# Performance work log

Hardware: AMD Instinct MI355X
Metric: run time of the kernel (lower is better)

Reference implementation:

```python
import jax, jax.numpy as jnp
import numpy as np

B, T, V, F, H, WIN = 512, 49, 34, 16, 64, 4
W = T - WIN + 1  # 46 sliding windows


def make_pe(max_len, d):
    pos = np.arange(max_len, dtype=np.float32)[:, None]
    div = np.exp(np.arange(0, d, 2, dtype=np.float32) * (-np.log(10000.0) / d))
    pe = np.zeros((max_len, d), dtype=np.float32)
    pe[:, 0::2] = np.sin(pos * div)
    pe[:, 1::2] = np.cos(pos * div)
    return jnp.asarray(pe)


def impute(arr, delta_ts, mask, w, b):
    # arr/mask [B,T,V], delta_ts [B,T]; serial masked cumulative-sum + LOCF scan
    missing = (mask == 0).astype(arr.dtype)
    dd = jnp.broadcast_to(delta_ts[:, :, None], arr.shape)

    def step(carry, inp):
        c_prev, x_prev = carry
        d_t, x_t, m_t = inp
        c_t = d_t + c_prev * m_t                      # cum delta resets at observations
        x_new = jnp.where(m_t > 0, x_prev, x_t)       # last-observation carry-forward
        return (c_t, x_new), (c_t, x_new)

    xs = (dd.swapaxes(0, 1)[1:], arr.swapaxes(0, 1)[1:], missing.swapaxes(0, 1)[1:])
    _, (c_rest, x_rest) = jax.lax.scan(step, (dd[:, 0], arr[:, 0]), xs)
    cum = jnp.concatenate([dd[:, :1], c_rest.swapaxes(0, 1)], axis=1)
    last = jnp.concatenate([arr[:, :1], x_rest.swapaxes(0, 1)], axis=1)
    cum = cum / jnp.max(cum)
    decay = jnp.exp(-jnp.clip(w * cum + b, 0.0, 1000.0))  # w,b broadcast [1,V]
    means = jnp.mean(arr, axis=1, keepdims=True)
    return arr * mask + (1 - mask) * (decay * last + (1 - decay) * means)


def gru_layer(x, Wih, Whh, bih, bhh):
    # torch GRU gate order r,z,n; Wih [in,3H], Whh [H,3H]
    nB = x.shape[0]
    Hh = Whh.shape[0]
    xW = x @ Wih + bih  # [B,T,3H] precomputed input projections

    def step(h, xw_t):
        gh = h @ Whh + bhh
        xr, xz, xn = jnp.split(xw_t, 3, axis=-1)
        hr, hz, hn = jnp.split(gh, 3, axis=-1)
        r = jax.nn.sigmoid(xr + hr)
        z = jax.nn.sigmoid(xz + hz)
        n = jnp.tanh(xn + r * hn)
        h_new = (1 - z) * n + z * h
        return h_new, h_new

    _, ys = jax.lax.scan(step, jnp.zeros((nB, Hh), x.dtype), xW.swapaxes(0, 1))
    return ys.swapaxes(0, 1)


def forward(arr, mask, time, w_input_decay, b_input_decay,
            enc_W1, enc_b1, enc_W2, enc_b2,
            tla_Wq, tla_bq, tla_Wk, tla_bk, tla_Wv, tla_bv,
            adj, mp_W1, mp_b1, mp_W2, mp_b2,
            sa_Wq, sa_bq, sa_Wk, sa_bk, sa_Wv, sa_bv,
            gru_Wih0, gru_Whh0, gru_bih0, gru_bhh0,
            gru_Wih1, gru_Whh1, gru_bih1, gru_bhh1,
            ta_Wq, ta_bq, ta_Wk, ta_bk, ta_Wv, ta_bv,
            cls_W1, cls_b1, cls_W2, cls_b2):
    tt = time.T  # [B,T]
    delta = jnp.concatenate([jnp.zeros((tt.shape[0], 1), tt.dtype), tt[:, 1:] - tt[:, :-1]], axis=1)
    x = impute(arr, delta, mask, w_input_decay, b_input_decay)  # [B,T,V]
    # per-variable 2-layer MLP encoders (batched over V via einsum)
    inp = jnp.stack([x, mask], axis=-1)  # [B,T,V,2]
    h = jax.nn.relu(jnp.einsum('btvi,vif->btvf', inp, enc_W1) + enc_b1)
    enc = jnp.einsum('btvf,vfg->btvg', h, enc_W2) + enc_b2  # [B,T,V,F]
    # sliding windows (torch unfold + permute) + window positional encoding
    idx = jnp.arange(W)[:, None] + jnp.arange(WIN)[None, :]
    win = enc[:, idx] + make_pe(WIN, F)[None, None, :, None, :]
    xw = win.reshape(B * W, WIN, V, F)
    # TimeLagAttentionLayer: separate attention per variable, batched via einsum
    q = jnp.einsum('blvf,vfg->blvg', xw, tla_Wq) + tla_bq
    k = jnp.einsum('blvf,vfg->blvg', xw, tla_Wk) + tla_bk
    v = jnp.einsum('blvf,vfg->blvg', xw, tla_Wv) + tla_bv
    scores = jnp.einsum('blvg,bmvg->bvlm', q, k) / jnp.sqrt(jnp.asarray(F, xw.dtype))
    att = jax.nn.softmax(scores, axis=-1)
    att_out = jnp.einsum('bvlm,bmvf->bvf', att, v)  # (att @ v) then sum over lag dim
    # MessagePassingLayer
    message = jnp.einsum('uv,bvf->buf', adj, att_out)
    mp_out = jax.nn.relu(message @ mp_W1 + mp_b1) @ mp_W2 + mp_b2  # [B*W,V,1] (t_out path)
    _ = mp_out
    latent = message
    l_out = latent.reshape(B, W, V, F).transpose(0, 2, 3, 1)  # [B,V,F,W]
    # SignalAttentionLayer (faithful: permute to [B,V,W,F] then raw reshape to [B*W,V,F])
    xs = l_out + make_pe(V, F)[None, :, :, None]
    xs = xs.transpose(0, 1, 3, 2).reshape(B * W, V, F)
    Q = xs @ sa_Wq + sa_bq
    K = xs @ sa_Wk + sa_bk
    Vv = xs @ sa_Wv + sa_bv
    sw = jax.nn.softmax(jnp.einsum('bnd,bmd->bnm', Q, K) / jnp.sqrt(jnp.asarray(F, xs.dtype)), axis=-1)
    s_out = jnp.einsum('bnm,bmd->bd', sw, Vv).reshape(B, W, F)  # (w @ V).sum(dim=1)
    # 2-layer GRU predictor
    g1 = gru_layer(s_out, gru_Wih0, gru_Whh0, gru_bih0, gru_bhh0)
    g2 = gru_layer(g1, gru_Wih1, gru_Whh1, gru_bih1, gru_bhh1)  # [B,W,H]
    # TemporalAttention pooling
    xt = g2 + make_pe(W, H)[None]
    Qt = xt @ ta_Wq + ta_bq
    Kt = xt @ ta_Wk + ta_bk
    Vt = xt @ ta_Wv + ta_bv
    tw = jax.nn.softmax(jnp.einsum('bld,bmd->blm', Qt, Kt) / jnp.sqrt(jnp.asarray(H, xt.dtype)), axis=-1)
    t_val = jnp.einsum('blm,bmd->bd', tw, Vt)  # [B,H]
    pred = jax.nn.relu(t_val @ cls_W1 + cls_b1) @ cls_W2 + cls_b2  # [B,1]
    return pred


def setup_inputs():
    key = jax.random.key(0)
    ks = jax.random.split(key, 48)

    def rn(k, shape, s=0.1):
        return jax.random.normal(k, shape, jnp.float32) * s

    d = {}
    d['arr'] = jax.random.normal(ks[0], (B, T, V), jnp.float32)
    d['mask'] = (jax.random.uniform(ks[1], (B, T, V)) < 0.7).astype(jnp.float32)
    d['time'] = jnp.cumsum(jax.random.uniform(ks[2], (T, B), jnp.float32), axis=0)
    d['w_input_decay'] = jnp.full((1, V), 0.1, jnp.float32)
    d['b_input_decay'] = jnp.zeros((1, V), jnp.float32)
    d['enc_W1'] = rn(ks[3], (V, 2, F), 0.5); d['enc_b1'] = rn(ks[4], (V, F))
    d['enc_W2'] = rn(ks[5], (V, F, F), 0.25); d['enc_b2'] = rn(ks[6], (V, F))
    d['tla_Wq'] = rn(ks[7], (V, F, F), 0.25); d['tla_bq'] = rn(ks[8], (V, F))
    d['tla_Wk'] = rn(ks[9], (V, F, F), 0.25); d['tla_bk'] = rn(ks[10], (V, F))
    d['tla_Wv'] = rn(ks[11], (V, F, F), 0.25); d['tla_bv'] = rn(ks[12], (V, F))
    d['adj'] = jnp.eye(V, dtype=jnp.float32) + 0.2 * jnp.ones((V, V), jnp.float32)
    d['mp_W1'] = rn(ks[13], (F, F), 0.25); d['mp_b1'] = rn(ks[14], (F,))
    d['mp_W2'] = rn(ks[15], (F, 1), 0.25); d['mp_b2'] = rn(ks[16], (1,))
    d['sa_Wq'] = rn(ks[17], (F, F), 0.25); d['sa_bq'] = rn(ks[18], (F,))
    d['sa_Wk'] = rn(ks[19], (F, F), 0.25); d['sa_bk'] = rn(ks[20], (F,))
    d['sa_Wv'] = rn(ks[21], (F, F), 0.25); d['sa_bv'] = rn(ks[22], (F,))
    d['gru_Wih0'] = rn(ks[23], (F, 3 * H), 0.2); d['gru_Whh0'] = rn(ks[24], (H, 3 * H), 0.1)
    d['gru_bih0'] = rn(ks[25], (3 * H,)); d['gru_bhh0'] = rn(ks[26], (3 * H,))
    d['gru_Wih1'] = rn(ks[27], (H, 3 * H), 0.1); d['gru_Whh1'] = rn(ks[28], (H, 3 * H), 0.1)
    d['gru_bih1'] = rn(ks[29], (3 * H,)); d['gru_bhh1'] = rn(ks[30], (3 * H,))
    d['ta_Wq'] = rn(ks[31], (H, H), 0.12); d['ta_bq'] = rn(ks[32], (H,))
    d['ta_Wk'] = rn(ks[33], (H, H), 0.12); d['ta_bk'] = rn(ks[34], (H,))
    d['ta_Wv'] = rn(ks[35], (H, H), 0.12); d['ta_bv'] = rn(ks[36], (H,))
    d['cls_W1'] = rn(ks[37], (H, H), 0.12); d['cls_b1'] = rn(ks[38], (H,))
    d['cls_W2'] = rn(ks[39], (H, 1), 0.12); d['cls_b2'] = rn(ks[40], (1,))
    return d


def reference(arr, mask, time, w_input_decay, b_input_decay,
              enc_W1, enc_b1, enc_W2, enc_b2,
              tla_Wq, tla_bq, tla_Wk, tla_bk, tla_Wv, tla_bv,
              adj, mp_W1, mp_b1, mp_W2, mp_b2,
              sa_Wq, sa_bq, sa_Wk, sa_bk, sa_Wv, sa_bv,
              gru_Wih0, gru_Whh0, gru_bih0, gru_bhh0,
              gru_Wih1, gru_Whh1, gru_bih1, gru_bhh1,
              ta_Wq, ta_bq, ta_Wk, ta_bk, ta_Wv, ta_bv,
              cls_W1, cls_b1, cls_W2, cls_b2):
    return forward(arr, mask, time, w_input_decay, b_input_decay,
                   enc_W1, enc_b1, enc_W2, enc_b2,
                   tla_Wq, tla_bq, tla_Wk, tla_bk, tla_Wv, tla_bv,
                   adj, mp_W1, mp_b1, mp_W2, mp_b2,
                   sa_Wq, sa_bq, sa_Wk, sa_bk, sa_Wv, sa_bv,
                   gru_Wih0, gru_Whh0, gru_bih0, gru_bhh0,
                   gru_Wih1, gru_Whh1, gru_bih1, gru_bhh1,
                   ta_Wq, ta_bq, ta_Wk, ta_bk, ta_Wv, ta_bv,
                   cls_W1, cls_b1, cls_W2, cls_b2)
```

## Files before the change

### kernel.cpp

```cpp
#include <hip/hip_runtime.h>
#include <math.h>

#define BB 512
#define TT 49
#define VV 34
#define FF 16
#define HH 64
#define WW 46
#define BW (BB*WW)
#define TH3 (3*HH)
#define ROWS 25088

#define SOUT_OFF   0ull
#define XW1_OFF    376832ull
#define G1_OFF     (XW1_OFF + 4521984ull)
#define XW2_OFF    (G1_OFF + 1507328ull)
#define G2_OFF     (XW2_OFF + 4521984ull)

#define MSG_SZ     12812288ull
#define CUM_SZ     852992ull
#define MEANS_SZ   17408ull
#define AO_OFF     12435456ull
#define MSG2_OFF   (AO_OFF + MSG_SZ)
#define CUM2_OFF   (MSG2_OFF + MSG_SZ)
#define LAST2_OFF  (CUM2_OFF + CUM_SZ)
#define MEANS2_OFF (LAST2_OFF + CUM_SZ)
#define MAX2_OFF   (MEANS2_OFF + MEANS_SZ)
#define PQ_OFF     (MAX2_OFF + 4ull)
#define SAW_OFF    (PQ_OFF + 6528ull)
#define FW_OFF     (SAW_OFF + 292ull)
#define WVIH_OFF   (FW_OFF + 27744ull)
#define BIAS2_OFF  (WVIH_OFF + 3072ull)

__global__ __launch_bounds__(256) void k_scan(
    const float* __restrict__ arr, const float* __restrict__ msk,
    const float* __restrict__ timeTB,
    float* __restrict__ cum, float* __restrict__ last,
    float* __restrict__ means, unsigned int* __restrict__ maxv) {
  int tid = blockIdx.x * 256 + threadIdx.x;
  int b = tid / VV, v = tid - b * VV;
  const int base = b * TT * VV + v;
  float x = arr[base];
  float c = 0.f, lm = 0.f, s = x;
  cum[base] = 0.f;
  last[base] = x;
  float tp = timeTB[b];
  for (int t = 1; t < TT; ++t) {
    float tc = timeTB[t * BB + b];
    float d = tc - tp; tp = tc;
    int e = base + t * VV;
    float a = arr[e], m = msk[e];
    float miss = (m == 0.f) ? 1.f : 0.f;
    c = d + c * miss;
    x = (miss > 0.f) ? x : a;
    cum[e] = c; last[e] = x;
    lm = fmaxf(lm, c);
    s += a;
  }
  means[tid] = s * (1.f / 49.f);
  #pragma unroll
  for (int off = 32; off; off >>= 1) lm = fmaxf(lm, __shfl_xor(lm, off));
  if ((threadIdx.x & 63) == 0) atomicMax(maxv, __float_as_uint(lm));
}

__global__ __launch_bounds__(256) void k_prep(
    const float* __restrict__ tlaWq, const float* __restrict__ tlaWk,
    const float* __restrict__ tlaWv,
    const float* __restrict__ tlaBq, const float* __restrict__ tlaBk,
    const float* __restrict__ tlaBv,
    const float* __restrict__ saWq, const float* __restrict__ saBq,
    const float* __restrict__ saWk, const float* __restrict__ saBk,
    const float* __restrict__ saWv, const float* __restrict__ saBv,
    const float* __restrict__ encW2, const float* __restrict__ encB2,
    const float* __restrict__ Wih0, const float* __restrict__ bih0,
    float* __restrict__ pqg, float* __restrict__ saw, float* __restrict__ fw,
    float* __restrict__ wvih, float* __restrict__ bias2) {
  const int bid = blockIdx.x;
  const int t = threadIdx.x;
  if (bid < 26) {
    int idx = bid * 256 + t;
    if (idx >= 6528) return;
    int which = idx / 2176;
    int r = idx - which * 2176;
    int l = r / 544;
    int rr = r - l * 544;
    int v = rr >> 4, f = rr & 15;
    const float* W = which == 0 ? tlaWq : which == 1 ? tlaWk : tlaWv;
    float acc = 0.f;
    #pragma unroll
    for (int i = 0; i < FF; ++i) {
      int i2 = i & ~1;
      float dv = expf(-logf(10000.f) * (float)i2 / (float)FF);
      float ang = (float)l * dv;
      float pe = (i & 1) ? cosf(ang) : sinf(ang);
      acc += pe * W[v * 256 + i * 16 + f];
    }
    pqg[idx] = acc;
  } else if (bid == 26) {
    int i = t & 15, j = t >> 4;
    float a = 0.f;
    #pragma unroll
    for (int f = 0; f < 16; ++f) a += saWq[i * 16 + f] * saWk[j * 16 + f];
    saw[j * 16 + i] = a;
    if (t < 16) {
      float pp = 0.f, qq = 0.f;
      #pragma unroll
      for (int f = 0; f < 16; ++f) { pp += saWq[t * 16 + f] * saBk[f]; qq += saWk[t * 16 + f] * saBq[f]; }
      saw[256 + t] = pp;
      saw[272 + t] = qq;
    }
    if (t == 0) {
      float c = 0.f;
      #pragma unroll
      for (int f = 0; f < 16; ++f) c += saBq[f] * saBk[f];
      saw[288] = c;
    }
  } else if (bid < 61) {
    const int v = bid - 27;
    const int f = t >> 4, o = t & 15;
    const float* W2v = encW2 + v * 256;
    float cq = 0.f, ck = 0.f, cv = 0.f;
    #pragma unroll
    for (int g = 0; g < 16; ++g) {
      float w2 = W2v[f * 16 + g];
      cq += w2 * tlaWq[v * 256 + g * 16 + o];
      ck += w2 * tlaWk[v * 256 + g * 16 + o];
      cv += w2 * tlaWv[v * 256 + g * 16 + o];
    }
    fw[v * 816 + 0 * 272 + f * 16 + o] = cq;
    fw[v * 816 + 1 * 272 + f * 16 + o] = ck;
    fw[v * 816 + 2 * 272 + f * 16 + o] = cv;
    if (t < 48) {
      int which = t >> 4, o2 = t & 15;
      const float* Wp = which == 0 ? tlaWq : which == 1 ? tlaWk : tlaWv;
      const float* Bp = which == 0 ? tlaBq : which == 1 ? tlaBk : tlaBv;
      float acc = Bp[v * 16 + o2];
      #pragma unroll
      for (int g = 0; g < 16; ++g) acc += encB2[v * 16 + g] * Wp[v * 256 + g * 16 + o2];
      fw[v * 816 + which * 272 + 256 + o2] = acc;
    }
  } else if (bid < 73) {
    int idx = (bid - 61) * 256 + t;
    int i = idx / 192, o = idx - i * 192;
    float acc = 0.f;
    #pragma unroll
    for (int f = 0; f < 16; ++f) acc += saWv[i * 16 + f] * Wih0[f * 192 + o];
    wvih[idx] = acc;
  } else {
    if (t < 192) {
      float acc = bih0[t];
      #pragma unroll
      for (int f = 0; f < 16; ++f) acc += 34.f * saBv[f] * Wih0[f * 192 + t];
      bias2[t] = acc;
    }
  }
}

__global__ __launch_bounds__(256) void k_enc4(
    const float* __restrict__ arr, const float* __restrict__ msk,
    const float* __restrict__ cum, const float* __restrict__ last,
    const float* __restrict__ means, const unsigned int* __restrict__ maxv,
    const float* __restrict__ wdec, const float* __restrict__ bdec,
    const float* __restrict__ W1, const float* __restrict__ B1,
    const float* __restrict__ fw, const float* __restrict__ pqg,
    float* __restrict__ ao) {
  __shared__ __align__(16) float pkv[4][3][TT * 20];
  const int v = blockIdx.x % VV;
  const int bgrp = blockIdx.x / VV;
  const int tid = threadIdx.x;
  const int wave = tid >> 6, lane = tid & 63;
  const int b = bgrp * 4 + wave;
  const float* fv = fw + v * 816;
  if (lane < TT) {
    const int t = lane;
    const int idx = (b * TT + t) * VV + v;
    float inv = 1.f / __uint_as_float(*maxv);
    float a = arr[idx], m = msk[idx];
    float cc = cum[idx] * inv;
    float ttc = fminf(fmaxf(wdec[v] * cc + bdec[v], 0.f), 1000.f);
    float dec = expf(-ttc);
    float xx = a * m + (1.f - m) * (dec * last[idx] + (1.f - dec) * means[b * VV + v]);
    float h[16];
    #pragma unroll
    for (int f = 0; f < 16; ++f)
      h[f] = fmaxf(xx * W1[v * 32 + f] + m * W1[v * 32 + 16 + f] + B1[v * 16 + f], 0.f);
    #pragma unroll
    for (int which = 0; which < 3; ++which) {
      const float* C = fv + which * 272;
      float ac[16];
      #pragma unroll
      for (int g = 0; g < 16; ++g) {
        float acc = C[256 + g];
        #pragma unroll
        for (int f = 0; f < 16; ++f) acc += h[f] * C[f * 16 + g];
        ac[g] = acc;
      }
      float4* dst = (float4*)&pkv[wave][which][t * 20];
      dst[0] = make_float4(ac[0], ac[1], ac[2], ac[3]);
      dst[1] = make_float4(ac[4], ac[5], ac[6], ac[7]);
      dst[2] = make_float4(ac[8], ac[9], ac[10], ac[11]);
      dst[3] = make_float4(ac[12], ac[13], ac[14], ac[15]);
    }
  }
  __syncthreads();
  if (lane < WW) {
    const int w = lane;
    const float* P = &pkv[wave][0][0];
    const float* K = &pkv[wave][1][0];
    const float* Vp = &pkv[wave][2][0];
    float kk[4][16];
    #pragma unroll
    for (int m = 0; m < 4; ++m) {
      const float4* Kr = (const float4*)&K[(w + m) * 20];
      float4 k0 = Kr[0], k1 = Kr[1], k2 = Kr[2], k3 = Kr[3];
      const float* pq = &pqg[2176 + m * 544 + v * 16];
      kk[m][0]=k0.x+pq[0]; kk[m][1]=k0.y+pq[1]; kk[m][2]=k0.z+pq[2]; kk[m][3]=k0.w+pq[3];
      kk[m][4]=k1.x+pq[4]; kk[m][5]=k1.y+pq[5]; kk[m][6]=k1.z+pq[6]; kk[m][7]=k1.w+pq[7];
      kk[m][8]=k2.x+pq[8]; kk[m][9]=k2.y+pq[9]; kk[m][10]=k2.z+pq[10]; kk[m][11]=k2.w+pq[11];
      kk[m][12]=k3.x+pq[12]; kk[m][13]=k3.y+pq[13]; kk[m][14]=k3.z+pq[14]; kk[m][15]=k3.w+pq[15];
    }
    float sc[4][4];
    #pragma unroll
    for (int l = 0; l < 4; ++l) {
      float qv[16];
      const float4* Pr = (const float4*)&P[(w + l) * 20];
      float4 p0 = Pr[0], p1 = Pr[1], p2 = Pr[2], p3 = Pr[3];
      const float* pq = &pqg[l * 544 + v * 16];
      qv[0]=p0.x+pq[0]; qv[1]=p0.y+pq[1]; qv[2]=p0.z+pq[2]; qv[3]=p0.w+pq[3];
      qv[4]=p1.x+pq[4]; qv[5]=p1.y+pq[5]; qv[6]=p1.z+pq[6]; qv[7]=p1.w+pq[7];
      qv[8]=p2.x+pq[8]; qv[9]=p2.y+pq[9]; qv[10]=p2.z+pq[10]; qv[11]=p2.w+pq[11];
      qv[12]=p3.x+pq[12]; qv[13]=p3.y+pq[13]; qv[14]=p3.z+pq[14]; qv[15]=p3.w+pq[15];
      #pragma unroll
      for (int m = 0; m < 4; ++m) {
        float s = 0.f;
        #pragma unroll
        for (int i = 0; i < 16; ++i) s += qv[i] * kk[m][i];
        sc[l][m] = s * 0.25f;
      }
    }
    float csum[4] = {0.f, 0.f, 0.f, 0.f};
    #pragma unroll
    for (int l = 0; l < 4; ++l) {
      float mx = fmaxf(fmaxf(sc[l][0], sc[l][1]), fmaxf(sc[l][2], sc[l][3]));
      float sum = 0.f;
      #pragma unroll
      for (int m = 0; m < 4; ++m) { sc[l][m] = expf(sc[l][m] - mx); sum += sc[l][m]; }
      float r = 1.f / sum;
      #pragma unroll
      for (int m = 0; m < 4; ++m) csum[m] += sc[l][m] * r;
    }
    float outv[16];
    #pragma unroll
    for (int f = 0; f < 16; ++f) outv[f] = 0.f;
    #pragma unroll
    for (int m = 0; m < 4; ++m) {
      float c = csum[m];
      const float4* Vr = (const float4*)&Vp[(w + m) * 20];
      float4 v0 = Vr[0], v1 = Vr[1], v2 = Vr[2], v3 = Vr[3];
      const float* pq = &pqg[2 * 2176 + m * 544 + v * 16];
      outv[0] += c*(v0.x+pq[0]); outv[1] += c*(v0.y+pq[1]); outv[2] += c*(v0.z+pq[2]); outv[3] += c*(v0.w+pq[3]);
      outv[4] += c*(v1.x+pq[4]); outv[5] += c*(v1.y+pq[5]); outv[6] += c*(v1.z+pq[6]); outv[7] += c*(v1.w+pq[7]);
      outv[8] += c*(v2.x+pq[8]); outv[9] += c*(v2.y+pq[9]); outv[10] += c*(v2.z+pq[10]); outv[11] += c*(v2.w+pq[11]);
      outv[12] += c*(v3.x+pq[12]); outv[13] += c*(v3.y+pq[13]); outv[14] += c*(v3.z+pq[14]); outv[15] += c*(v3.w+pq[15]);
    }
    float4* d4 = (float4*)(ao + ((size_t)(b * VV + v) * WW + w) * 16);
    #pragma unroll
    for (int j = 0; j < 4; ++j)
      d4[j] = make_float4(outv[4*j], outv[4*j+1], outv[4*j+2], outv[4*j+3]);
  }
}

#define MPW 12
__global__ __launch_bounds__(256) void k_mp(
    const float* __restrict__ ao, const float* __restrict__ adj,
    float* __restrict__ msg2) {
  __shared__ float adjs[VV * VV];
  __shared__ __align__(16) float aos[VV][MPW * 16];
  __shared__ float pes[VV * 16];
  const int bb = blockIdx.x >> 2;
  const int wt = blockIdx.x & 3;
  const int w0 = wt * MPW;
  const int wc = (wt == 3) ? (WW - 3 * MPW) : MPW;
  const int tid = threadIdx.x;
  for (int i = tid; i < VV * VV; i += 256) adjs[i] = adj[i];
  for (int i = tid; i < VV * 16; i += 256) {
    int u = i >> 4, f = i & 15;
    int f2 = f & ~1;
    float dv = expf(-logf(10000.f) * (float)f2 / 16.f);
    float ang = (float)u * dv;
    pes[i] = (f & 1) ? cosf(ang) : sinf(ang);
  }
  const int nq = wc * 4;
  for (int i = tid; i < VV * nq; i += 256) {
    int vv2 = i / nq, r = i - vv2 * nq;
    int wl = r >> 2, q = r & 3;
    float4 val = *(const float4*)(ao + ((size_t)(bb * VV + vv2) * WW + w0 + wl) * 16 + q * 4);
    *(float4*)&aos[vv2][wl * 16 + q * 4] = val;
  }
  __syncthreads();
  for (int i = tid; i < VV * nq; i += 256) {
    int u = i / nq, r = i - u * nq;
    int wl = r >> 2, q = r & 3;
    float a0 = 0.f, a1 = 0.f, a2 = 0.f, a3 = 0.f;
    for (int vv2 = 0; vv2 < VV; ++vv2) {
      float a = adjs[u * VV + vv2];
      float4 s = *(const float4*)&aos[vv2][wl * 16 + q * 4];
      a0 += a * s.x; a1 += a * s.y; a2 += a * s.z; a3 += a * s.w;
    }
    float4 o = make_float4(a0 + pes[u * 16 + q * 4],
                           a1 + pes[u * 16 + q * 4 + 1],
                           a2 + pes[u * 16 + q * 4 + 2],
                           a3 + pes[u * 16 + q * 4 + 3]);
    *(float4*)(msg2 + ((size_t)(bb * VV + u) * WW + w0 + wl) * 16 + q * 4) = o;
  }
}

#define RL(x,i) __uint_as_float(__builtin_amdgcn_readlane(__float_as_uint(x), (i)))
__global__ __launch_bounds__(256) void k_sa6(
    const float* __restrict__ msg2, const float* __restrict__ saw,
    const float* __restrict__ wvih, const float* __restrict__ bias2,
    float* __restrict__ xw1) {
  __shared__ __align__(16) float xs[4][VV * 20];
  __shared__ float esc[4][VV * 35];
  __shared__ float csL[4][VV];
  __shared__ __align__(16) float ybL[4][16];
  const int tid = threadIdx.x;
  const int g = tid >> 6, lane = tid & 63;
  const int n = blockIdx.x * 4 + g;
  {
    const float4* src = (const float4*)(msg2 + (size_t)blockIdx.x * 4 * 544);
    for (int i = tid; i < 544; i += 256) {
      int gg = i / 136, r = i - gg * 136;
      int m = r >> 2, q = r & 3;
      ((float4*)&xs[gg][m * 20])[q] = src[i];
    }
  }
  __syncthreads();
  float x[16];
  float w = 0.f;
  if (lane < VV) {
    const float4* xr = (const float4*)&xs[g][lane * 20];
    float4 a0 = xr[0], a1 = xr[1], a2 = xr[2], a3 = xr[3];
    x[0]=a0.x; x[1]=a0.y; x[2]=a0.z; x[3]=a0.w;
    x[4]=a1.x; x[5]=a1.y; x[6]=a1.z; x[7]=a1.w;
    x[8]=a2.x; x[9]=a2.y; x[10]=a2.z; x[11]=a2.w;
    x[12]=a3.x; x[13]=a3.y; x[14]=a3.z; x[15]=a3.w;
    float z[16];
    float u = 0.f;
    #pragma unroll
    for (int j = 0; j < 16; ++j) {
      float acc = 0.f;
      #pragma unroll
      for (int i = 0; i < 16; ++i) acc += saw[j * 16 + i] * x[i];
      z[j] = acc;
    }
    #pragma unroll
    for (int i = 0; i < 16; ++i) { u += saw[256 + i] * x[i]; w += saw[272 + i] * x[i]; }
    const float c0 = saw[288] + u;
    float e[VV];
    #pragma unroll
    for (int m = 0; m < VV; ++m) {
      float p0 = 0.f, p1 = 0.f, p2 = 0.f, p3 = 0.f;
      #pragma unroll
      for (int i = 0; i < 16; i += 4) {
        p0 += z[i]     * RL(x[i], m);
        p1 += z[i + 1] * RL(x[i + 1], m);
        p2 += z[i + 2] * RL(x[i + 2], m);
        p3 += z[i + 3] * RL(x[i + 3], m);
      }
      e[m] = (((p0 + p1) + (p2 + p3)) + RL(w, m) + c0) * 0.25f;
    }
    float mx = e[0];
    #pragma unroll
    for (int m = 1; m < VV; ++m) mx = fmaxf(mx, e[m]);
    float sum = 0.f;
    #pragma unroll
    for (int m = 0; m < VV; ++m) { e[m] = expf(e[m] - mx); sum += e[m]; }
    float rr = 1.f / sum;
    #pragma unroll
    for (int m = 0; m < VV; ++m) esc[g][lane * 35 + m] = e[m] * rr;
  }
  __syncthreads();
  if (lane < VV) {
    float cs = 0.f;
    #pragma unroll
    for (int l = 0; l < VV; ++l) cs += esc[g][l * 35 + lane];
    csL[g][lane] = cs;
  }
  __syncthreads();
  if (lane < 16) {
    float acc = 0.f;
    #pragma unroll
    for (int m = 0; m < VV; ++m) acc += csL[g][m] * xs[g][m * 20 + lane];
    ybL[g][lane] = acc;
  }
  __syncthreads();
  {
    const float4* yr = (const float4*)&ybL[g][0];
    float4 y0 = yr[0], y1 = yr[1], y2 = yr[2], y3 = yr[3];
    float yv[16];
    yv[0]=y0.x; yv[1]=y0.y; yv[2]=y0.z; yv[3]=y0.w;
    yv[4]=y1.x; yv[5]=y1.y; yv[6]=y1.z; yv[7]=y1.w;
    yv[8]=y2.x; yv[9]=y2.y; yv[10]=y2.z; yv[11]=y2.w;
    yv[12]=y3.x; yv[13]=y3.y; yv[14]=y3.z; yv[15]=y3.w;
    #pragma unroll
    for (int k = 0; k < 3; ++k) {
      int o = lane + k * 64;
      float acc = bias2[o];
      #pragma unroll
      for (int i = 0; i < 16; ++i) acc += yv[i] * wvih[i * 192 + o];
      xw1[(size_t)n * 192 + o] = acc;
    }
  }
}

__global__ __launch_bounds__(64) void k_gru2(
    const float* __restrict__ xw, const float* __restrict__ Whh,
    const float* __restrict__ bhh, float* __restrict__ gout) {
  const int tid = threadIdx.x;
  const int b = blockIdx.x;
  float wr[64], wz[64], wn[64];
  #pragma unroll
  for (int i = 0; i < 64; ++i) {
    wr[i] = Whh[i * 192 + tid];
    wz[i] = Whh[i * 192 + 64 + tid];
    wn[i] = Whh[i * 192 + 128 + tid];
  }
  const float br = bhh[tid], bz = bhh[64 + tid], bn = bhh[128 + tid];
  float h = 0.f;
  const float* xr = xw + (size_t)b * WW * 192;
  for (int w = 0; w < WW; ++w, xr += 192) {
    float xrv = xr[tid], xzv = xr[64 + tid], xnv = xr[128 + tid];
    float pr0 = br, pr1 = 0.f, pr2 = 0.f, pr3 = 0.f;
    float pz0 = bz, pz1 = 0.f, pz2 = 0.f, pz3 = 0.f;
    float pn0 = bn, pn1 = 0.f, pn2 = 0.f, pn3 = 0.f;
    #pragma unroll
    for (int i = 0; i < 64; i += 4) {
      float h0 = RL(h, i), h1 = RL(h, i + 1), h2 = RL(h, i + 2), h3 = RL(h, i + 3);
      pr0 += h0 * wr[i];     pr1 += h1 * wr[i + 1];
      pr2 += h2 * wr[i + 2]; pr3 += h3 * wr[i + 3];
      pz0 += h0 * wz[i];     pz1 += h1 * wz[i + 1];
      pz2 += h2 * wz[i + 2]; pz3 += h3 * wz[i + 3];
      pn0 += h0 * wn[i];     pn1 += h1 * wn[i + 1];
      pn2 += h2 * wn[i + 2]; pn3 += h3 * wn[i + 3];
    }
    float ar = (pr0 + pr1) + (pr2 + pr3);
    float az = (pz0 + pz1) + (pz2 + pz3);
    float an = (pn0 + pn1) + (pn2 + pn3);
    float r = 1.f / (1.f + expf(-(xrv + ar)));
    float z = 1.f / (1.f + expf(-(xzv + az)));
    float n = tanhf(xnv + r * an);
    h = (1.f - z) * n + z * h;
    gout[((size_t)b * WW + w) * HH + tid] = h;
  }
}

__global__ __launch_bounds__(192) void k_xw2(
    const float* __restrict__ x, const float* __restrict__ Wih,
    const float* __restrict__ bih, float* __restrict__ xw) {
  __shared__ float xsh[16][HH];
  int n0 = blockIdx.x * 16;
  int tid = threadIdx.x;
  for (int idx = tid; idx < 16 * HH; idx += 192) {
    int ns = idx >> 6, i = idx & 63;
    xsh[ns][i] = x[(size_t)(n0 + ns) * HH + i];
  }
  __syncthreads();
  float acc[16];
  float bb = bih[tid];
  #pragma unroll
  for (int ns = 0; ns < 16; ++ns) acc[ns] = bb;
  for (int i = 0; i < HH; ++i) {
    float wv = Wih[i * TH3 + tid];
    #pragma unroll
    for (int ns = 0; ns < 16; ++ns) acc[ns] += xsh[ns][i] * wv;
  }
  #pragma unroll
  for (int ns = 0; ns < 16; ++ns) xw[(size_t)(n0 + ns) * TH3 + tid] = acc[ns];
}

__global__ __launch_bounds__(256) void k_ta(
    const float* __restrict__ g2,
    const float* __restrict__ Wq, const float* __restrict__ bq,
    const float* __restrict__ Wk, const float* __restrict__ bk,
    const float* __restrict__ Wv, const float* __restrict__ bv,
    const float* __restrict__ cW1, const float* __restrict__ cb1,
    const float* __restrict__ cW2, const float* __restrict__ cb2,
    float* __restrict__ out) {
  __shared__ float xt[WW * 65];
  __shared__ float QKVs[3][WW * 65];
  __shared__ float sc[WW * WW];
  __shared__ float cs[WW];
  __shared__ float tval[HH];
  __shared__ float hrelu[HH];
  int tid = threadIdx.x;
  int b = blockIdx.x;
  for (int idx = tid; idx < WW * HH; idx += 256) {
    int w = idx >> 6, d = idx & 63;
    int f2 = d & ~1;
    float dv = expf(-logf(10000.f) * (float)f2 / (float)HH);
    float ang = (float)w * dv;
    float pe = (d & 1) ? cosf(ang) : sinf(ang);
    xt[w * 65 + d] = g2[(size_t)(b * WW + w) * HH + d] + pe;
  }
  __syncthreads();
  if (tid < 192) {
    int which = tid >> 6, d = tid & 63;
    const float* Wt = which == 0 ? Wq : which == 1 ? Wk : Wv;
    float bias = (which == 0 ? bq : which == 1 ? bk : bv)[d];
    float col[HH];
    #pragma unroll
    for (int i = 0; i < HH; ++i) col[i] = Wt[i * HH + d];
    float* dst = &QKVs[which][0];
    for (int w = 0; w < WW; ++w) {
      float acc = bias;
      #pragma unroll
      for (int i = 0; i < HH; ++i) acc += xt[w * 65 + i] * col[i];
      dst[w * 65 + d] = acc;
    }
  }
  __syncthreads();
  for (int idx = tid; idx < WW * WW; idx += 256) {
    int l = idx / WW, m = idx - l * WW;
    float s = 0.f;
    #pragma unroll
    for (int i = 0; i < HH; ++i) s += QKVs[0][l * 65 + i] * QKVs[1][m * 65 + i];
    sc[idx] = s * 0.125f;
  }
  __syncthreads();
  if (tid < WW) {
    float mx = -1e30f;
    for (int m = 0; m < WW; ++m) mx = fmaxf(mx, sc[tid * WW + m]);
    float sum = 0.f;
    for (int m = 0; m < WW; ++m) { float e = expf(sc[tid * WW + m] - mx); sc[tid * WW + m] = e; sum += e; }
    float r = 1.f / sum;
    for (int m = 0; m < WW; ++m) sc[tid * WW + m] *= r;
  }
  __syncthreads();
  if (tid < WW) {
    float s = 0.f;
    for (int l = 0; l < WW; ++l) s += sc[l * WW + tid];
    cs[tid] = s;
  }
  __syncthreads();
  if (tid < HH) {
    float acc = 0.f;
    for (int m = 0; m < WW; ++m) acc += cs[m] * QKVs[2][m * 65 + tid];
    tval[tid] = acc;
  }
  __syncthreads();
  if (tid < HH) {
    float acc = cb1[tid];
    #pragma unroll
    for (int d = 0; d < HH; ++d) acc += tval[d] * cW1[d * HH + tid];
    hrelu[tid] = fmaxf(acc, 0.f);
  }
  __syncthreads();
  if (tid == 0) {
    float acc = cb2[0];
    for (int j = 0; j < HH; ++j) acc += hrelu[j] * cW2[j];
    out[b] = acc;
  }
}

extern "C" void kernel_launch(void* const* d_in, const int* in_sizes, int n_in,
                              void* d_out, int out_size, void* d_ws, size_t ws_size,
                              hipStream_t stream) {
  (void)in_sizes; (void)n_in; (void)out_size; (void)ws_size;
  const float* arr    = (const float*)d_in[0];
  const float* msk    = (const float*)d_in[1];
  const float* timeTB = (const float*)d_in[2];
  const float* wdec   = (const float*)d_in[3];
  const float* bdec   = (const float*)d_in[4];
  const float* encW1  = (const float*)d_in[5];
  const float* encB1  = (const float*)d_in[6];
  const float* encW2  = (const float*)d_in[7];
  const float* encB2  = (const float*)d_in[8];
  const float* tlaWq  = (const float*)d_in[9];
  const float* tlaBq  = (const float*)d_in[10];
  const float* tlaWk  = (const float*)d_in[11];
  const float* tlaBk  = (const float*)d_in[12];
  const float* tlaWv  = (const float*)d_in[13];
  const float* tlaBv  = (const float*)d_in[14];
  const float* adj    = (const float*)d_in[15];
  const float* saWq   = (const float*)d_in[20];
  const float* saBq   = (const float*)d_in[21];
  const float* saWk   = (const float*)d_in[22];
  const float* saBk   = (const float*)d_in[23];
  const float* saWv   = (const float*)d_in[24];
  const float* saBv   = (const float*)d_in[25];
  const float* gWih0  = (const float*)d_in[26];
  const float* gWhh0  = (const float*)d_in[27];
  const float* gBih0  = (const float*)d_in[28];
  const float* gBhh0  = (const float*)d_in[29];
  const float* gWih1  = (const float*)d_in[30];
  const float* gWhh1  = (const float*)d_in[31];
  const float* gBih1  = (const float*)d_in[32];
  const float* gBhh1  = (const float*)d_in[33];
  const float* taWq   = (const float*)d_in[34];
  const float* taBq   = (const float*)d_in[35];
  const float* taWk   = (const float*)d_in[36];
  const float* taBk   = (const float*)d_in[37];
  const float* taWv   = (const float*)d_in[38];
  const float* taBv   = (const float*)d_in[39];
  const float* cW1    = (const float*)d_in[40];
  const float* cb1    = (const float*)d_in[41];
  const float* cW2    = (const float*)d_in[42];
  const float* cb2    = (const float*)d_in[43];
  float* out = (float*)d_out;
  float* ws  = (float*)d_ws;

  float* ao    = ws + AO_OFF;
  float* msg2  = ws + MSG2_OFF;
  float* cum   = ws + CUM2_OFF;
  float* last  = ws + LAST2_OFF;
  float* means = ws + MEANS2_OFF;
  unsigned int* maxv = (unsigned int*)(ws + MAX2_OFF);
  float* pqg   = ws + PQ_OFF;
  float* saw   = ws + SAW_OFF;
  float* fw    = ws + FW_OFF;
  float* wvih  = ws + WVIH_OFF;
  float* bias2 = ws + BIAS2_OFF;

  float* xw1  = ws + XW1_OFF;
  float* g1   = ws + G1_OFF;
  float* xw2  = ws + XW2_OFF;
  float* g2   = ws + G2_OFF;

  hipMemsetAsync(maxv, 0, sizeof(unsigned int), stream);
  k_scan<<<68, 256, 0, stream>>>(arr, msk, timeTB, cum, last, means, maxv);
  k_prep<<<74, 256, 0, stream>>>(tlaWq, tlaWk, tlaWv, tlaBq, tlaBk, tlaBv,
                                 saWq, saBq, saWk, saBk, saWv, saBv,
                                 encW2, encB2, gWih0, gBih0,
                                 pqg, saw, fw, wvih, bias2);
  k_enc4<<<VV * 128, 256, 0, stream>>>(arr, msk, cum, last, means, maxv,
                                       wdec, bdec, encW1, encB1, fw, pqg, ao);
  k_mp<<<BB * 4, 256, 0, stream>>>(ao, adj, msg2);
  k_sa6<<<BW / 4, 256, 0, stream>>>(msg2, saw, wvih, bias2, xw1);
  k_gru2<<<BB, 64, 0, stream>>>(xw1, gWhh0, gBhh0, g1);
  k_xw2<<<BW / 16, 192, 0, stream>>>(g1, gWih1, gBih1, xw2);
  k_gru2<<<BB, 64, 0, stream>>>(xw2, gWhh1, gBhh1, g2);
  k_ta<<<BB, 256, 0, stream>>>(g2, taWq, taBq, taWk, taBk, taWv, taBv,
                               cW1, cb1, cW2, cb2, out);
}
```

Measured before the change: 345.8 us.

## Register-tile adjacency matmul, use LDS in self-attention, fast GRU activations

Message passing now transposes and pads the adjacency matrix in shared memory so each thread computes a 4x4 block of outputs, reusing both loaded operands across four accumulators. The self-attention kernel drops the readlane broadcast in favour of float4 reads from shared memory, plus an extra barrier to share per-node terms. The GRU kernel replaces expf/tanhf with __expf-based sigmoid and tanh. These aim to cut shared-memory traffic and transcendental cost, at a small cost in accuracy and some lost parallelism in the message-passing loop.

```diff
diff --git a/kernel.cpp b/kernel.cpp
--- a/kernel.cpp
+++ b/kernel.cpp
@@ -31,6 +31,13 @@
 #define FW_OFF     (SAW_OFF + 292ull)
 #define WVIH_OFF   (FW_OFF + 27744ull)
 #define BIAS2_OFF  (WVIH_OFF + 3072ull)
+
+#define RL(x,i) __uint_as_float(__builtin_amdgcn_readlane(__float_as_uint(x), (i)))
+__device__ __forceinline__ float fsig(float x) { return 1.f / (1.f + __expf(-x)); }
+__device__ __forceinline__ float ftanh(float x) {
+  float t = __expf(2.f * x);
+  return 1.f - 2.f / (t + 1.f);
+}
 
 __global__ __launch_bounds__(256) void k_scan(
     const float* __restrict__ arr, const float* __restrict__ msk,
@@ -271,10 +278,10 @@
 }
 
 #define MPW 12
-__global__ __launch_bounds__(256) void k_mp(
+__global__ __launch_bounds__(256) void k_mp2(
     const float* __restrict__ ao, const float* __restrict__ adj,
     float* __restrict__ msg2) {
-  __shared__ float adjs[VV * VV];
+  __shared__ __align__(16) float adjT[VV][36];
   __shared__ __align__(16) float aos[VV][MPW * 16];
   __shared__ float pes[VV * 16];
   const int bb = blockIdx.x >> 2;
@@ -282,7 +289,10 @@
   const int w0 = wt * MPW;
   const int wc = (wt == 3) ? (WW - 3 * MPW) : MPW;
   const int tid = threadIdx.x;
-  for (int i = tid; i < VV * VV; i += 256) adjs[i] = adj[i];
+  for (int i = tid; i < VV * 36; i += 256) {
+    int vv2 = i / 36, u = i - vv2 * 36;
+    adjT[vv2][u] = (u < VV) ? adj[u * VV + vv2] : 0.f;
+  }
   for (int i = tid; i < VV * 16; i += 256) {
     int u = i >> 4, f = i & 15;
     int f2 = f & ~1;
@@ -298,30 +308,43 @@
     *(float4*)&aos[vv2][wl * 16 + q * 4] = val;
   }
   __syncthreads();
-  for (int i = tid; i < VV * nq; i += 256) {
-    int u = i / nq, r = i - u * nq;
+  for (int item = tid; item < 9 * nq; item += 256) {
+    int utile = item / nq;
+    int r = item - utile * nq;
     int wl = r >> 2, q = r & 3;
-    float a0 = 0.f, a1 = 0.f, a2 = 0.f, a3 = 0.f;
+    float acc[4][4];
+    #pragma unroll
+    for (int a = 0; a < 4; ++a)
+      #pragma unroll
+      for (int c = 0; c < 4; ++c) acc[a][c] = 0.f;
     for (int vv2 = 0; vv2 < VV; ++vv2) {
-      float a = adjs[u * VV + vv2];
-      float4 s = *(const float4*)&aos[vv2][wl * 16 + q * 4];
-      a0 += a * s.x; a1 += a * s.y; a2 += a * s.z; a3 += a * s.w;
-    }
-    float4 o = make_float4(a0 + pes[u * 16 + q * 4],
-                           a1 + pes[u * 16 + q * 4 + 1],
-                           a2 + pes[u * 16 + q * 4 + 2],
-                           a3 + pes[u * 16 + q * 4 + 3]);
-    *(float4*)(msg2 + ((size_t)(bb * VV + u) * WW + w0 + wl) * 16 + q * 4) = o;
-  }
-}
-
-#define RL(x,i) __uint_as_float(__builtin_amdgcn_readlane(__float_as_uint(x), (i)))
-__global__ __launch_bounds__(256) void k_sa6(
+      float4 av = *(const float4*)&adjT[vv2][utile * 4];
+      float4 sv = *(const float4*)&aos[vv2][wl * 16 + q * 4];
+      acc[0][0] += av.x * sv.x; acc[0][1] += av.x * sv.y; acc[0][2] += av.x * sv.z; acc[0][3] += av.x * sv.w;
+      acc[1][0] += av.y * sv.x; acc[1][1] += av.y * sv.y; acc[1][2] += av.y * sv.z; acc[1][3] += av.y * sv.w;
+      acc[2][0] += av.z * sv.x; acc[2][1] += av.z * sv.y; acc[2][2] += av.z * sv.z; acc[2][3] += av.z * sv.w;
+      acc[3][0] += av.w * sv.x; acc[3][1] += av.w * sv.y; acc[3][2] += av.w * sv.z; acc[3][3] += av.w * sv.w;
+    }
+    #pragma unroll
+    for (int a = 0; a < 4; ++a) {
+      int u = utile * 4 + a;
+      if (u < VV) {
+        const float* pe = &pes[u * 16 + q * 4];
+        float4 o = make_float4(acc[a][0] + pe[0], acc[a][1] + pe[1],
+                               acc[a][2] + pe[2], acc[a][3] + pe[3]);
+        *(float4*)(msg2 + ((size_t)(bb * VV + u) * WW + w0 + wl) * 16 + q * 4) = o;
+      }
+    }
+  }
+}
+
+__global__ __launch_bounds__(256) void k_sa5(
     const float* __restrict__ msg2, const float* __restrict__ saw,
     const float* __restrict__ wvih, const float* __restrict__ bias2,
     float* __restrict__ xw1) {
   __shared__ __align__(16) float xs[4][VV * 20];
   __shared__ float esc[4][VV * 35];
+  __shared__ float wsL[4][VV];
   __shared__ float csL[4][VV];
   __shared__ __align__(16) float ybL[4][16];
   const int tid = threadIdx.x;
@@ -336,17 +359,16 @@
     }
   }
   __syncthreads();
-  float x[16];
-  float w = 0.f;
+  float z[16];
+  float u = 0.f;
   if (lane < VV) {
+    float x[16];
     const float4* xr = (const float4*)&xs[g][lane * 20];
     float4 a0 = xr[0], a1 = xr[1], a2 = xr[2], a3 = xr[3];
     x[0]=a0.x; x[1]=a0.y; x[2]=a0.z; x[3]=a0.w;
     x[4]=a1.x; x[5]=a1.y; x[6]=a1.z; x[7]=a1.w;
     x[8]=a2.x; x[9]=a2.y; x[10]=a2.z; x[11]=a2.w;
     x[12]=a3.x; x[13]=a3.y; x[14]=a3.z; x[15]=a3.w;
-    float z[16];
-    float u = 0.f;
     #pragma unroll
     for (int j = 0; j < 16; ++j) {
       float acc = 0.f;
@@ -354,21 +376,24 @@
       for (int i = 0; i < 16; ++i) acc += saw[j * 16 + i] * x[i];
       z[j] = acc;
     }
+    float w = 0.f;
     #pragma unroll
     for (int i = 0; i < 16; ++i) { u += saw[256 + i] * x[i]; w += saw[272 + i] * x[i]; }
-    const float c0 = saw[288] + u;
+    wsL[g][lane] = w;
+  }
+  __syncthreads();
+  if (lane < VV) {
+    const float c0 = saw[288];
     float e[VV];
     #pragma unroll
     for (int m = 0; m < VV; ++m) {
-      float p0 = 0.f, p1 = 0.f, p2 = 0.f, p3 = 0.f;
-      #pragma unroll
-      for (int i = 0; i < 16; i += 4) {
-        p0 += z[i]     * RL(x[i], m);
-        p1 += z[i + 1] * RL(x[i + 1], m);
-        p2 += z[i + 2] * RL(x[i + 2], m);
-        p3 += z[i + 3] * RL(x[i + 3], m);
-      }
-      e[m] = (((p0 + p1) + (p2 + p3)) + RL(w, m) + c0) * 0.25f;
+      const float4* xm = (const float4*)&xs[g][m * 20];
+      float4 b0 = xm[0], b1 = xm[1], b2 = xm[2], b3 = xm[3];
+      float p0 = z[0]*b0.x + z[1]*b0.y + z[2]*b0.z + z[3]*b0.w;
+      float p1 = z[4]*b1.x + z[5]*b1.y + z[6]*b1.z + z[7]*b1.w;
+      float p2 = z[8]*b2.x + z[9]*b2.y + z[10]*b2.z + z[11]*b2.w;
+      float p3 = z[12]*b3.x + z[13]*b3.y + z[14]*b3.z + z[15]*b3.w;
+      e[m] = (((p0 + p1) + (p2 + p3)) + u + wsL[g][m] + c0) * 0.25f;
     }
     float mx = e[0];
     #pragma unroll
@@ -447,9 +472,9 @@
     float ar = (pr0 + pr1) + (pr2 + pr3);
     float az = (pz0 + pz1) + (pz2 + pz3);
     float an = (pn0 + pn1) + (pn2 + pn3);
-    float r = 1.f / (1.f + expf(-(xrv + ar)));
-    float z = 1.f / (1.f + expf(-(xzv + az)));
-    float n = tanhf(xnv + r * an);
+    float r = fsig(xrv + ar);
+    float z = fsig(xzv + az);
+    float n = ftanh(xnv + r * an);
     h = (1.f - z) * n + z * h;
     gout[((size_t)b * WW + w) * HH + tid] = h;
   }
@@ -635,8 +660,8 @@
                                  pqg, saw, fw, wvih, bias2);
   k_enc4<<<VV * 128, 256, 0, stream>>>(arr, msk, cum, last, means, maxv,
                                        wdec, bdec, encW1, encB1, fw, pqg, ao);
-  k_mp<<<BB * 4, 256, 0, stream>>>(ao, adj, msg2);
-  k_sa6<<<BW / 4, 256, 0, stream>>>(msg2, saw, wvih, bias2, xw1);
+  k_mp2<<<BB * 4, 256, 0, stream>>>(ao, adj, msg2);
+  k_sa5<<<BW / 4, 256, 0, stream>>>(msg2, saw, wvih, bias2, xw1);
   k_gru2<<<BB, 64, 0, stream>>>(xw1, gWhh0, gBhh0, g1);
   k_xw2<<<BW / 16, 192, 0, stream>>>(g1, gWih1, gBih1, xw2);
   k_gru2<<<BB, 64, 0, stream>>>(xw2, gWhh1, gBhh1, g2);
```

New measurement: 382.5 us. +10.6%, slower.
